# Performance work log

Hardware: AMD Instinct MI355X
Metric: run time of the kernel (lower is better)

The kernel has to match this reference:

```python
import jax, jax.numpy as jnp
import numpy as np

EPS = 1e-08


def setup_inputs() -> dict:
    key = jax.random.key(0)
    k1, k2, k3 = jax.random.split(key, 3)
    b, c, s = 4, 128, 32
    oc, k = 128, 3
    x = jax.random.normal(k1, (b, c, s, s, s), dtype=jnp.float32)
    y = jax.random.normal(k2, (b, c), dtype=jnp.float32)
    weight = jax.random.normal(k3, (oc, c, k, k, k), dtype=jnp.float32)
    return {"x": x, "y": y, "weight": weight}


def reference(x, y, weight):
    b, c, h, w, d = x.shape
    oc, ic, kh, kw, kd = weight.shape
    # modulate: per-sample scale of input channels
    ws = weight[None] * y[:, None, :, None, None, None]  # (b, oc, ic, k, k, k)
    # demodulate
    demod = jax.lax.rsqrt(jnp.sum(jnp.square(ws), axis=(2, 3, 4, 5)) + EPS)  # (b, oc)
    ws = ws * demod[:, :, None, None, None, None]
    # grouped conv: fold batch into channels, groups=b
    xr = x.reshape(1, b * c, h, w, d)
    wr = ws.reshape(b * oc, ic, kh, kw, kd)
    # same padding for stride=1, dilation=1: (k-1)//2
    pad = (kh - 1) // 2
    out = jax.lax.conv_general_dilated(
        xr, wr,
        window_strides=(1, 1, 1),
        padding=[(pad, pad)] * 3,
        feature_group_count=b,
        dimension_numbers=("NCDHW", "OIDHW", "NCDHW"),
    )
    return out.reshape(b, oc, h, w, d)
```

## Files before the change

### kernel.cpp

```cpp
#include <hip/hip_runtime.h>
#include <hip/hip_bf16.h>

typedef __attribute__((ext_vector_type(8))) short bf16x8;
typedef __attribute__((ext_vector_type(4))) float f32x4;
typedef unsigned short u16;
typedef unsigned int u32;

#define NP 34
#define XT_BYTES ((size_t)4 * NP * NP * NP * 128 * 2)

__device__ __forceinline__ u16 f2bf(float f) {
  __hip_bfloat16 h = __float2bfloat16(f);
  return __builtin_bit_cast(u16, h);
}

__device__ __forceinline__ void gload_lds16(const u16* g, u16* l) {
  __builtin_amdgcn_global_load_lds(
      (const __attribute__((address_space(1))) u32*)g,
      (__attribute__((address_space(3))) u32*)l, 16, 0, 0);
}

#define WAITV(N) asm volatile("s_waitcnt vmcnt(" #N ")" ::: "memory")
#define BAR() do { __builtin_amdgcn_s_barrier(); asm volatile("" ::: "memory"); } while (0)

__global__ __launch_bounds__(128) void kmodw(const float* __restrict__ w,
                                             const float* __restrict__ y,
                                             u16* __restrict__ wmod) {
  const int oc = blockIdx.x, b = blockIdx.y;
  const int ic = threadIdx.x;
  const float* wp = w + (oc * 128 + ic) * 27;
  float wv[27];
  float s = 0.f;
#pragma unroll
  for (int t = 0; t < 27; ++t) { wv[t] = wp[t]; s += wv[t] * wv[t]; }
  const float yv = y[b * 128 + ic];
  float v = yv * yv * s;
#pragma unroll
  for (int m = 1; m < 64; m <<= 1) v += __shfl_xor(v, m);
  __shared__ float part[2];
  const int lane = ic & 63, wid = ic >> 6;
  if (lane == 0) part[wid] = v;
  __syncthreads();
  const float demod = rsqrtf(part[0] + part[1] + 1e-8f);
  const float sc = yv * demod;
#pragma unroll
  for (int t = 0; t < 27; ++t)
    wmod[((b * 27 + t) * 128 + oc) * 128 + ic] = f2bf(wv[t] * sc);
}

__global__ __launch_bounds__(128) void khalo(u16* __restrict__ xt) {
  const int zy = blockIdx.x, b = blockIdx.y;
  const int zz = zy / NP, yy = zy % NP;
  u16* row = xt + ((size_t)((b * NP + zz) * NP + yy) * NP) * 128;
  u32* wp = (u32*)row;
  if (zz == 0 || zz == NP - 1 || yy == 0 || yy == NP - 1) {
#pragma unroll
    for (int i = 0; i < 17; ++i) wp[i * 128 + threadIdx.x] = 0;
  } else {
    if (threadIdx.x < 64) wp[threadIdx.x] = 0;
    else ((u32*)(row + 33 * 128))[threadIdx.x - 64] = 0;
  }
}

__global__ __launch_bounds__(256) void kcastx(const float* __restrict__ x,
                                              u16* __restrict__ xt) {
  const int yq = blockIdx.x, z = blockIdx.y, b = blockIdx.z;
  const int tid = threadIdx.x;
  __shared__ u16 t[32 * 132];
  const float* xp = x + (size_t)b * 128 * 32768 + (z * 32 + yq) * 32;
#pragma unroll
  for (int p = 0; p < 16; ++p) {
    const int ic = p * 8 + (tid >> 5), xx = tid & 31;
    t[xx * 132 + ic] = f2bf(xp[(size_t)ic * 32768 + xx]);
  }
  __syncthreads();
  u16* xtb = xt + (((size_t)(b * NP + z + 1) * NP + (yq + 1)) * NP + 1) * 128;
#pragma unroll
  for (int p = 0; p < 4; ++p) {
    const int xx = p * 8 + (tid >> 5), icq = tid & 31;
    *(ushort4*)(xtb + (size_t)xx * 128 + icq * 4) = *(const ushort4*)&t[xx * 132 + icq * 4];
  }
}

__global__ __launch_bounds__(256, 2) void kconv(const u16* __restrict__ xt,
                                                const u16* __restrict__ wmod,
                                                float* __restrict__ out) {
  __shared__ __align__(16) u16 Asm[2][8192];
  __shared__ __align__(16) u16 Bsm[22528];
  const int tid = threadIdx.x;
  const int lane = tid & 63, wn = tid >> 6;
  const int l15 = lane & 15, sgq = lane >> 4;
  const int bid = blockIdx.x;
  const int wgid = ((bid & 7) << 6) + (bid >> 3);
  const int b = wgid >> 7, yt = (wgid >> 5) & 3, z = wgid & 31;
  const int y0 = yt << 3;

  const u16* wb = wmod + (size_t)b * 27 * 16384;
  const u16* xb = xt + (size_t)b * (NP * NP * NP) * 128;

  f32x4 acc[8][4];
#pragma unroll
  for (int i = 0; i < 8; ++i)
#pragma unroll
    for (int j = 0; j < 4; ++j) acc[i][j] = (f32x4){0.f, 0.f, 0.f, 0.f};

  const int aoc0 = tid >> 3, aj = tid & 7;
  const u16* asrc = wb + (aoc0 << 7) + ((aj ^ (aoc0 & 7)) << 3);
  const int adst = tid << 3;
  int sybase[4], xp0[4];
#pragma unroll
  for (int nf = 0; nf < 4; ++nf) {
    sybase[nf] = (((wn << 1) + (nf >> 1)) + 1) * 2176;
    xp0[nf] = ((nf & 1) << 4) + l15 + 1;
  }
  const int kswz0 = sgq ^ (l15 & 7);

  auto stageA = [&](int ks1) {
    const int g1 = ks1 / 9, j1 = ks1 - g1 * 9;
    const int tap = (g1 >> 1) * 9 + j1, hh = g1 & 1;
    const u16* base = asrc + tap * 16384 + (hh << 6);
    u16* dst = &Asm[ks1 & 1][adst];
#pragma unroll
    for (int k = 0; k < 4; ++k)
      gload_lds16(base + (k << 12), dst + (k << 11));
  };
  auto stageB = [&](int g) {
    const int dz = (g >> 1) - 1, hh = g & 1;
    const int zro = (z + 1 + dz) * NP + y0;
#pragma unroll
    for (int r = 0; r < 11; ++r) {
      int s = r * 256 + tid;
      const int dst = s << 3;
      s = s < 2719 ? s : 2719;
      const int sy = s / 272;
      const int rem = s - sy * 272;
      const int xpos = rem >> 3, j = rem & 7;
      gload_lds16(xb + (size_t)((zro + sy) * NP + xpos) * 128 + (hh << 6) +
                      ((j ^ (xpos & 7)) << 3),
                  &Bsm[dst]);
    }
  };
  auto ldAf = [&](bf16x8* af, int par, int mh, int kswz) {
    const u16* Ah = &Asm[par][0];
#pragma unroll
    for (int mm = 0; mm < 4; ++mm) {
      const int oc = (mh << 6) + (mm << 4) + l15;
      af[mm] = *(const bf16x8*)&Ah[(oc << 6) + (kswz << 3)];
    }
  };
  auto ldBv = [&](bf16x8* bv, int kk, int dy, int dx) {
#pragma unroll
    for (int nf = 0; nf < 4; ++nf) {
      const int xp = xp0[nf] + dx;
      const int off = sybase[nf] + dy * 2176 + (xp << 6) +
                      ((((kk << 2) + sgq) ^ (xp & 7)) << 3);
      bv[nf] = *(const bf16x8*)&Bsm[off];
    }
  };

  bf16x8 af0[4], af1[4], bv0[4], bv1[4];

#define MFMA16(MH, AF, BV)                                                 \
  { __builtin_amdgcn_s_setprio(1);                                         \
    _Pragma("unroll") for (int mm = 0; mm < 4; ++mm)                       \
      _Pragma("unroll") for (int nf = 0; nf < 4; ++nf)                     \
        acc[(MH) * 4 + mm][nf] = __builtin_amdgcn_mfma_f32_16x16x32_bf16(  \
            (AF)[mm], (BV)[nf], acc[(MH) * 4 + mm][nf], 0, 0, 0);          \
    __builtin_amdgcn_s_setprio(0); }

  stageB(0);
  stageA(0);
  WAITV(0); BAR();

  for (int g = 0; g < 6; ++g) {
    for (int j = 0; j < 9; ++j) {
      const int ks = g * 9 + j;
      const int par = ks & 1;
      const int dy = j / 3 - 1, dx = (j % 3) - 1;
      if (ks < 53) stageA(ks + 1);
      ldAf(af0, par, 0, kswz0);
      ldBv(bv0, 0, dy, dx);
      MFMA16(0, af0, bv0);
      ldAf(af1, par, 1, kswz0);
      MFMA16(1, af1, bv0);
      ldAf(af0, par, 0, kswz0 ^ 4);
      ldBv(bv1, 1, dy, dx);
      MFMA16(0, af0, bv1);
      ldAf(af1, par, 1, kswz0 ^ 4);
      MFMA16(1, af1, bv1);
      if (j == 8) {
        if (g < 5) {
          BAR();
          stageB(g + 1);
          WAITV(0); BAR();
        }
      } else {
        WAITV(0); BAR();
      }
    }
  }

#pragma unroll
  for (int m = 0; m < 8; ++m) {
    const int ocb = (m << 4) + (sgq << 2);
#pragma unroll
    for (int nf = 0; nf < 4; ++nf) {
      const int n = (wn << 6) + (nf << 4) + l15;
      const int yy = n >> 5, xx = n & 31;
      float* op = out + ((size_t)(b * 128 + ocb) << 15) + (z << 10) +
                  ((y0 + yy) << 5) + xx;
#pragma unroll
      for (int r = 0; r < 4; ++r) op[(size_t)r << 15] = acc[m][nf][r];
    }
  }
#undef MFMA16
}

extern "C" void kernel_launch(void* const* d_in, const int* in_sizes, int n_in,
                              void* d_out, int out_size, void* d_ws, size_t ws_size,
                              hipStream_t stream) {
  const float* x = (const float*)d_in[0];
  const float* y = (const float*)d_in[1];
  const float* w = (const float*)d_in[2];
  float* out = (float*)d_out;
  u16* xt = (u16*)d_ws;
  u16* wmod = (u16*)((char*)d_ws + XT_BYTES);

  hipLaunchKernelGGL(khalo, dim3(NP * NP, 4), dim3(128), 0, stream, xt);
  hipLaunchKernelGGL(kmodw, dim3(128, 4), dim3(128), 0, stream, w, y, wmod);
  hipLaunchKernelGGL(kcastx, dim3(32, 32, 4), dim3(256), 0, stream, x, xt);
  hipLaunchKernelGGL(kconv, dim3(512), dim3(256), 0, stream, xt, wmod, out);
}
```

Baseline: 119.0 us.

## Use two waves per conv block with larger per-wave 128x128 output tiles

The conv kernel drops from 256 to 128 threads per block. Each wave now computes all 128 output channels across 128 spatial positions (8x8 MFMA tiles), so A and B fragment loads are reused across more MFMAs. Staging loops are doubled so the two waves can still fill LDS. The risk is heavy register pressure from 256 accumulator floats per lane, fewer waves to hide latency, and more load instructions per thread.

```diff
diff --git a/kernel.cpp b/kernel.cpp
--- a/kernel.cpp
+++ b/kernel.cpp
@@ -82,7 +82,7 @@
   }
 }
 
-__global__ __launch_bounds__(256, 2) void kconv(const u16* __restrict__ xt,
+__global__ __launch_bounds__(128, 1) void kconv(const u16* __restrict__ xt,
                                                 const u16* __restrict__ wmod,
                                                 float* __restrict__ out) {
   __shared__ __align__(16) u16 Asm[2][8192];
@@ -98,20 +98,21 @@
   const u16* wb = wmod + (size_t)b * 27 * 16384;
   const u16* xb = xt + (size_t)b * (NP * NP * NP) * 128;
 
-  f32x4 acc[8][4];
+  f32x4 acc[8][8];
 #pragma unroll
   for (int i = 0; i < 8; ++i)
 #pragma unroll
-    for (int j = 0; j < 4; ++j) acc[i][j] = (f32x4){0.f, 0.f, 0.f, 0.f};
+    for (int j = 0; j < 8; ++j) acc[i][j] = (f32x4){0.f, 0.f, 0.f, 0.f};
 
   const int aoc0 = tid >> 3, aj = tid & 7;
   const u16* asrc = wb + (aoc0 << 7) + ((aj ^ (aoc0 & 7)) << 3);
   const int adst = tid << 3;
-  int sybase[4], xp0[4];
-#pragma unroll
-  for (int nf = 0; nf < 4; ++nf) {
-    sybase[nf] = (((wn << 1) + (nf >> 1)) + 1) * 2176;
-    xp0[nf] = ((nf & 1) << 4) + l15 + 1;
+  int sybase[8], xp0[8];
+#pragma unroll
+  for (int nf = 0; nf < 8; ++nf) {
+    const int n = (wn << 7) + (nf << 4) + l15;
+    sybase[nf] = ((n >> 5) + 1) * 2176;
+    xp0[nf] = (n & 31) + 1;
   }
   const int kswz0 = sgq ^ (l15 & 7);
 
@@ -121,15 +122,15 @@
     const u16* base = asrc + tap * 16384 + (hh << 6);
     u16* dst = &Asm[ks1 & 1][adst];
 #pragma unroll
-    for (int k = 0; k < 4; ++k)
-      gload_lds16(base + (k << 12), dst + (k << 11));
+    for (int k = 0; k < 8; ++k)
+      gload_lds16(base + (k << 11), dst + (k << 10));
   };
   auto stageB = [&](int g) {
     const int dz = (g >> 1) - 1, hh = g & 1;
     const int zro = (z + 1 + dz) * NP + y0;
 #pragma unroll
-    for (int r = 0; r < 11; ++r) {
-      int s = r * 256 + tid;
+    for (int r = 0; r < 22; ++r) {
+      int s = (r << 7) + tid;
       const int dst = s << 3;
       s = s < 2719 ? s : 2719;
       const int sy = s / 272;
@@ -140,17 +141,17 @@
                   &Bsm[dst]);
     }
   };
-  auto ldAf = [&](bf16x8* af, int par, int mh, int kswz) {
+  auto ldAf = [&](bf16x8* af, int par, int kswz) {
     const u16* Ah = &Asm[par][0];
 #pragma unroll
-    for (int mm = 0; mm < 4; ++mm) {
-      const int oc = (mh << 6) + (mm << 4) + l15;
-      af[mm] = *(const bf16x8*)&Ah[(oc << 6) + (kswz << 3)];
+    for (int m = 0; m < 8; ++m) {
+      const int oc = (m << 4) + l15;
+      af[m] = *(const bf16x8*)&Ah[(oc << 6) + (kswz << 3)];
     }
   };
   auto ldBv = [&](bf16x8* bv, int kk, int dy, int dx) {
 #pragma unroll
-    for (int nf = 0; nf < 4; ++nf) {
+    for (int nf = 0; nf < 8; ++nf) {
       const int xp = xp0[nf] + dx;
       const int off = sybase[nf] + dy * 2176 + (xp << 6) +
                       ((((kk << 2) + sgq) ^ (xp & 7)) << 3);
@@ -158,14 +159,14 @@
     }
   };
 
-  bf16x8 af0[4], af1[4], bv0[4], bv1[4];
-
-#define MFMA16(MH, AF, BV)                                                 \
+  bf16x8 af[8], bv[8];
+
+#define MFMA64()                                                           \
   { __builtin_amdgcn_s_setprio(1);                                         \
-    _Pragma("unroll") for (int mm = 0; mm < 4; ++mm)                       \
-      _Pragma("unroll") for (int nf = 0; nf < 4; ++nf)                     \
-        acc[(MH) * 4 + mm][nf] = __builtin_amdgcn_mfma_f32_16x16x32_bf16(  \
-            (AF)[mm], (BV)[nf], acc[(MH) * 4 + mm][nf], 0, 0, 0);          \
+    _Pragma("unroll") for (int mm = 0; mm < 8; ++mm)                       \
+      _Pragma("unroll") for (int nf = 0; nf < 8; ++nf)                     \
+        acc[mm][nf] = __builtin_amdgcn_mfma_f32_16x16x32_bf16(             \
+            af[mm], bv[nf], acc[mm][nf], 0, 0, 0);                         \
     __builtin_amdgcn_s_setprio(0); }
 
   stageB(0);
@@ -178,16 +179,12 @@
       const int par = ks & 1;
       const int dy = j / 3 - 1, dx = (j % 3) - 1;
       if (ks < 53) stageA(ks + 1);
-      ldAf(af0, par, 0, kswz0);
-      ldBv(bv0, 0, dy, dx);
-      MFMA16(0, af0, bv0);
-      ldAf(af1, par, 1, kswz0);
-      MFMA16(1, af1, bv0);
-      ldAf(af0, par, 0, kswz0 ^ 4);
-      ldBv(bv1, 1, dy, dx);
-      MFMA16(0, af0, bv1);
-      ldAf(af1, par, 1, kswz0 ^ 4);
-      MFMA16(1, af1, bv1);
+      ldAf(af, par, kswz0);
+      ldBv(bv, 0, dy, dx);
+      MFMA64();
+      ldAf(af, par, kswz0 ^ 4);
+      ldBv(bv, 1, dy, dx);
+      MFMA64();
       if (j == 8) {
         if (g < 5) {
           BAR();
@@ -204,8 +201,8 @@
   for (int m = 0; m < 8; ++m) {
     const int ocb = (m << 4) + (sgq << 2);
 #pragma unroll
-    for (int nf = 0; nf < 4; ++nf) {
-      const int n = (wn << 6) + (nf << 4) + l15;
+    for (int nf = 0; nf < 8; ++nf) {
+      const int n = (wn << 7) + (nf << 4) + l15;
       const int yy = n >> 5, xx = n & 31;
       float* op = out + ((size_t)(b * 128 + ocb) << 15) + (z << 10) +
                   ((y0 + yy) << 5) + xx;
@@ -213,7 +210,7 @@
       for (int r = 0; r < 4; ++r) op[(size_t)r << 15] = acc[m][nf][r];
     }
   }
-#undef MFMA16
+#undef MFMA64
 }
 
 extern "C" void kernel_launch(void* const* d_in, const int* in_sizes, int n_in,
@@ -229,5 +226,5 @@
   hipLaunchKernelGGL(khalo, dim3(NP * NP, 4), dim3(128), 0, stream, xt);
   hipLaunchKernelGGL(kmodw, dim3(128, 4), dim3(128), 0, stream, w, y, wmod);
   hipLaunchKernelGGL(kcastx, dim3(32, 32, 4), dim3(256), 0, stream, x, xt);
-  hipLaunchKernelGGL(kconv, dim3(512), dim3(256), 0, stream, xt, wmod, out);
-}
+  hipLaunchKernelGGL(kconv, dim3(512), dim3(128), 0, stream, xt, wmod, out);
+}
```

Result: slower. 136.2 us (+14.4%).
